# Performance work log

Hardware: AMD Instinct MI355X
Metric: run time of the kernel (lower is better)

## Reference

```python
import jax, jax.numpy as jnp
import numpy as np

EMBED_DIM = 1024
NUM_HEADS = 16
HEAD_DIM = EMBED_DIM // NUM_HEADS
FEATURE_EPS = 1e-06
DEN_EPS = 1e-06


def setup_inputs() -> dict:
    key = jax.random.key(0)
    k_x, k_qw, k_qb, k_ow, k_ob = jax.random.split(key, 5)
    b, l = 2, 2048
    x = jax.random.normal(k_x, (b, l, EMBED_DIM), dtype=jnp.float32)
    s = 1.0 / np.sqrt(EMBED_DIM)
    qkv_w = jax.random.uniform(k_qw, (3 * EMBED_DIM, EMBED_DIM), minval=-s, maxval=s, dtype=jnp.float32)
    qkv_b = jax.random.uniform(k_qb, (3 * EMBED_DIM,), minval=-s, maxval=s, dtype=jnp.float32)
    out_w = jax.random.uniform(k_ow, (EMBED_DIM, EMBED_DIM), minval=-s, maxval=s, dtype=jnp.float32)
    out_b = jax.random.uniform(k_ob, (EMBED_DIM,), minval=-s, maxval=s, dtype=jnp.float32)
    return {"x": x, "qkv_w": qkv_w, "qkv_b": qkv_b, "out_w": out_w, "out_b": out_b}


def reference(x, qkv_w, qkv_b, out_w, out_b):
    b, l, e = x.shape
    # qkv projection -> (3, b, h, l, d)
    qkv = (x @ qkv_w.T + qkv_b).reshape(b, l, 3, NUM_HEADS, HEAD_DIM)
    qkv = jnp.transpose(qkv, (2, 0, 3, 1, 4))
    q, k, v = qkv[0], qkv[1], qkv[2]
    # phi(x) = relu(x) + eps
    q = jax.nn.relu(q) + FEATURE_EPS
    k = jax.nn.relu(k) + FEATURE_EPS
    # running outer-product state: (b, h, l, d, d)
    kv = jnp.cumsum(jnp.einsum('bhld,bhle->bhlde', k, v), axis=2)
    k_cum = jnp.cumsum(k, axis=2)
    num = jnp.einsum('bhld,bhlde->bhle', q, kv)
    den = jnp.maximum(jnp.einsum('bhld,bhld->bhl', q, k_cum)[..., None], DEN_EPS)
    out = num / den  # (b, h, l, d)
    out = jnp.transpose(out, (0, 2, 1, 3)).reshape(b, l, e)
    return out @ out_w.T + out_b
```

## Files before the change

### kernel.cpp

```cpp
#include <hip/hip_runtime.h>
#include <hip/hip_bf16.h>
#include <cstdint>

#define B_ 2
#define L_ 2048
#define E_ 1024
#define H_ 16
#define D_ 64
#define N3_ 3072
#define NCHUNK 32
#define CHUNK 64

typedef __attribute__((ext_vector_type(8))) short bf16x8;
typedef __attribute__((ext_vector_type(4))) float f32x4;

__device__ __forceinline__ unsigned short f2bf(float f) {
  unsigned u = __float_as_uint(f);
  unsigned r = (u + 0x7fffu + ((u >> 16) & 1u)) >> 16;
  return (unsigned short)r;
}

__global__ __launch_bounds__(256) void k_cvt_bf16(const float* __restrict__ src,
                                                  unsigned short* __restrict__ dst,
                                                  int n4) {
  const int i = blockIdx.x * 256 + threadIdx.x;
  if (i < n4) {
    float4 v = reinterpret_cast<const float4*>(src)[i];
    ushort4 o;
    o.x = f2bf(v.x); o.y = f2bf(v.y); o.z = f2bf(v.z); o.w = f2bf(v.w);
    reinterpret_cast<ushort4*>(dst)[i] = o;
  }
}

template <int EPI>
__global__ __launch_bounds__(256) void k_mfma_gemm(
    const unsigned short* __restrict__ A,
    const unsigned short* __restrict__ Bm,
    const float* __restrict__ bias,
    float* __restrict__ O,
    unsigned short* __restrict__ Qb, unsigned short* __restrict__ Kb,
    unsigned short* __restrict__ Vb, const int K) {
  __shared__ short As[128 * 32];
  __shared__ short Bs[128 * 32];
  const int tid = threadIdx.x;
  const int lane = tid & 63;
  const int wave = tid >> 6;
  const int wr = wave >> 1, wc = wave & 1;
  const int m0 = blockIdx.y * 128, n0 = blockIdx.x * 128;
  const int srow = tid >> 2;
  const int scol = (tid & 3) << 3;
  f32x4 acc[4][4];
#pragma unroll
  for (int i = 0; i < 4; ++i)
#pragma unroll
    for (int j = 0; j < 4; ++j) acc[i][j] = (f32x4){0.f, 0.f, 0.f, 0.f};

  const int l15 = lane & 15, l16 = lane >> 4;
  const int aoff0 = (wr * 64 + l15) * 32 + l16 * 8;
  const int boff0 = (wc * 64 + l15) * 32 + l16 * 8;

  for (int k0 = 0; k0 < K; k0 += 32) {
    const short* gA = (const short*)&A[(size_t)(m0 + srow) * K + k0 + scol];
    const short* gB = (const short*)&Bm[(size_t)(n0 + srow) * K + k0 + scol];
    __builtin_amdgcn_global_load_lds(
        (const __attribute__((address_space(1))) unsigned int*)gA,
        (__attribute__((address_space(3))) unsigned int*)&As[tid * 8], 16, 0, 0);
    __builtin_amdgcn_global_load_lds(
        (const __attribute__((address_space(1))) unsigned int*)(gA + (size_t)64 * K),
        (__attribute__((address_space(3))) unsigned int*)&As[2048 + tid * 8], 16, 0, 0);
    __builtin_amdgcn_global_load_lds(
        (const __attribute__((address_space(1))) unsigned int*)gB,
        (__attribute__((address_space(3))) unsigned int*)&Bs[tid * 8], 16, 0, 0);
    __builtin_amdgcn_global_load_lds(
        (const __attribute__((address_space(1))) unsigned int*)(gB + (size_t)64 * K),
        (__attribute__((address_space(3))) unsigned int*)&Bs[2048 + tid * 8], 16, 0, 0);
    __syncthreads();
    bf16x8 af[4], bfr[4];
#pragma unroll
    for (int f = 0; f < 4; ++f)
      af[f] = *reinterpret_cast<const bf16x8*>(&As[aoff0 + f * 16 * 32]);
#pragma unroll
    for (int f = 0; f < 4; ++f)
      bfr[f] = *reinterpret_cast<const bf16x8*>(&Bs[boff0 + f * 16 * 32]);
#pragma unroll
    for (int m = 0; m < 4; ++m)
#pragma unroll
      for (int n = 0; n < 4; ++n)
        acc[m][n] = __builtin_amdgcn_mfma_f32_16x16x32_bf16(af[m], bfr[n], acc[m][n], 0, 0, 0);
    __syncthreads();
  }

  const int rbase = l16 * 4;
#pragma unroll
  for (int m = 0; m < 4; ++m) {
#pragma unroll
    for (int n = 0; n < 4; ++n) {
      const int col = n0 + wc * 64 + n * 16 + l15;
      const float bv = bias[col];
#pragma unroll
      for (int j = 0; j < 4; ++j) {
        const int row = m0 + wr * 64 + m * 16 + rbase + j;
        const float val = acc[m][n][j] + bv;
        if (EPI == 0) {
          const int b = row >> 11, l = row & 2047;
          const int t = col >> 10, hd = col & 1023;
          const int h = hd >> 6, d = hd & 63;
          const size_t dst = (((size_t)(b * 16 + h)) * 2048 + l) * 64 + d;
          if (t == 0)      Qb[dst] = f2bf(fmaxf(val, 0.f) + 1e-6f);
          else if (t == 1) Kb[dst] = f2bf(fmaxf(val, 0.f) + 1e-6f);
          else             Vb[dst] = f2bf(val);
        } else {
          O[(size_t)row * 1024 + col] = val;
        }
      }
    }
  }
}

__global__ __launch_bounds__(128) void k_chunkB(
    const unsigned short* __restrict__ Kb, const unsigned short* __restrict__ Vb,
    float* __restrict__ ST, unsigned short* __restrict__ Vtb) {
  __shared__ __align__(16) unsigned short Kt[64 * 72];
  __shared__ __align__(16) unsigned short Vt[64 * 72];
  const int tid = threadIdx.x;
  const int lane = tid & 63, w = tid >> 6;
  const int c = lane & 15, g = lane >> 4;
  const int bid = blockIdx.x;
  const int bh = bid >> 5, ch = bid & 31;
  const size_t base = ((size_t)bh * L_ + (size_t)ch * CHUNK) * D_;
  const int l = tid >> 1, hf = tid & 1;
  bf16x8 kv[4], vv[4];
#pragma unroll
  for (int i = 0; i < 4; ++i) {
    kv[i] = *reinterpret_cast<const bf16x8*>(&Kb[base + (size_t)l * 64 + hf * 32 + i * 8]);
    vv[i] = *reinterpret_cast<const bf16x8*>(&Vb[base + (size_t)l * 64 + hf * 32 + i * 8]);
  }
#pragma unroll
  for (int i = 0; i < 4; ++i)
#pragma unroll
    for (int r = 0; r < 8; ++r) {
      const int d = hf * 32 + i * 8 + r;
      Kt[d * 72 + l] = (unsigned short)kv[i][r];
      Vt[d * 72 + l] = (unsigned short)vv[i][r];
    }
  __syncthreads();
  bf16x8 kf[4][2], vf[2][2];
#pragma unroll
  for (int dt = 0; dt < 4; ++dt)
#pragma unroll
    for (int kh = 0; kh < 2; ++kh)
      kf[dt][kh] = *reinterpret_cast<const bf16x8*>(&Kt[(dt * 16 + c) * 72 + g * 8 + kh * 32]);
#pragma unroll
  for (int ei = 0; ei < 2; ++ei)
#pragma unroll
    for (int kh = 0; kh < 2; ++kh)
      vf[ei][kh] = *reinterpret_cast<const bf16x8*>(&Vt[((w * 2 + ei) * 16 + c) * 72 + g * 8 + kh * 32]);
  f32x4 acc[2][4];
#pragma unroll
  for (int ei = 0; ei < 2; ++ei)
#pragma unroll
    for (int dt = 0; dt < 4; ++dt) acc[ei][dt] = (f32x4){0.f, 0.f, 0.f, 0.f};
#pragma unroll
  for (int ei = 0; ei < 2; ++ei)
#pragma unroll
    for (int dt = 0; dt < 4; ++dt)
#pragma unroll
      for (int kh = 0; kh < 2; ++kh)
        acc[ei][dt] = __builtin_amdgcn_mfma_f32_16x16x32_bf16(vf[ei][kh], kf[dt][kh], acc[ei][dt], 0, 0, 0);
  const size_t stbase = (size_t)bid * 5120;
#pragma unroll
  for (int ei = 0; ei < 2; ++ei)
#pragma unroll
    for (int dt = 0; dt < 4; ++dt)
#pragma unroll
      for (int r = 0; r < 4; ++r)
        ST[stbase + (size_t)((w * 2 + ei) * 16 + 4 * g + r) * 64 + dt * 16 + c] = acc[ei][dt][r];
#pragma unroll
  for (int ei = 0; ei < 2; ++ei)
#pragma unroll
    for (int kh = 0; kh < 2; ++kh)
      *reinterpret_cast<bf16x8*>(&Vtb[(size_t)bid * 4096 + ((w * 2 + ei) * 16 + c) * 64 + g * 8 + kh * 32]) = vf[ei][kh];
  if (w == 0) {
    const short one = (c == 0) ? (short)0x3F80 : (short)0;
    bf16x8 of;
#pragma unroll
    for (int r = 0; r < 8; ++r) of[r] = one;
    f32x4 az[4];
#pragma unroll
    for (int dt = 0; dt < 4; ++dt) az[dt] = (f32x4){0.f, 0.f, 0.f, 0.f};
#pragma unroll
    for (int dt = 0; dt < 4; ++dt)
#pragma unroll
      for (int kh = 0; kh < 2; ++kh)
        az[dt] = __builtin_amdgcn_mfma_f32_16x16x32_bf16(of, kf[dt][kh], az[dt], 0, 0, 0);
    if (g == 0) {
#pragma unroll
      for (int dt = 0; dt < 4; ++dt)
        ST[stbase + 64 * 64 + dt * 16 + c] = az[dt][0];
    }
  }
}

__global__ __launch_bounds__(256) void k_prefix2(const float* __restrict__ ST,
                                                 unsigned short* __restrict__ STb) {
  const int bh = blockIdx.x;
  const int tid = threadIdx.x;
  float run[16];
#pragma unroll
  for (int j = 0; j < 16; ++j) run[j] = 0.f;
  for (int cc = 0; cc < NCHUNK; ++cc) {
    const size_t base = ((size_t)bh * NCHUNK + cc) * 5120;
    const float* p = ST + base + (size_t)tid * 16;
    unsigned short* qo = STb + base + (size_t)tid * 16;
#pragma unroll
    for (int j4 = 0; j4 < 4; ++j4) {
      float4 t = *reinterpret_cast<const float4*>(&p[j4 * 4]);
      ushort4 o;
      o.x = f2bf(run[j4 * 4 + 0]); o.y = f2bf(run[j4 * 4 + 1]);
      o.z = f2bf(run[j4 * 4 + 2]); o.w = f2bf(run[j4 * 4 + 3]);
      *reinterpret_cast<ushort4*>(&qo[j4 * 4]) = o;
      run[j4 * 4 + 0] += t.x; run[j4 * 4 + 1] += t.y;
      run[j4 * 4 + 2] += t.z; run[j4 * 4 + 3] += t.w;
    }
  }
  if (tid < 64) {
    float rz = 0.f;
    for (int cc = 0; cc < NCHUNK; ++cc) {
      const size_t base = ((size_t)bh * NCHUNK + cc) * 5120 + 4096 + tid;
      float t = ST[base];
      STb[base] = f2bf(rz);
      rz += t;
    }
  }
}

__global__ __launch_bounds__(256) void k_chunkD(
    const unsigned short* __restrict__ Qb, const unsigned short* __restrict__ Kb,
    const unsigned short* __restrict__ Vtb, const unsigned short* __restrict__ STb,
    unsigned short* __restrict__ attnb) {
  __shared__ __align__(16) unsigned short P[4][1024];
  const int tid = threadIdx.x;
  const int lane = tid & 63, lt = tid >> 6;
  const int c = lane & 15, g = lane >> 4;
  const int bid = blockIdx.x;
  const int bh = bid >> 5, ch = bid & 31;
  const int b = bh >> 4, h = bh & 15;
  const size_t qkbase = ((size_t)bh * L_ + (size_t)ch * CHUNK) * D_;
  bf16x8 q[2], k4[4][2], s[5][2], vt[4][2], pa[2];
#pragma unroll
  for (int kh = 0; kh < 2; ++kh)
    q[kh] = *reinterpret_cast<const bf16x8*>(&Qb[qkbase + (size_t)(lt * 16 + c) * 64 + g * 8 + kh * 32]);
#pragma unroll
  for (int jt = 0; jt < 4; ++jt)
#pragma unroll
    for (int kh = 0; kh < 2; ++kh)
      k4[jt][kh] = *reinterpret_cast<const bf16x8*>(&Kb[qkbase + (size_t)(jt * 16 + c) * 64 + g * 8 + kh * 32]);
  const size_t stbase = (size_t)bid * 5120;
#pragma unroll
  for (int et = 0; et < 5; ++et)
#pragma unroll
    for (int kh = 0; kh < 2; ++kh)
      s[et][kh] = *reinterpret_cast<const bf16x8*>(&STb[stbase + (size_t)(et * 16 + c) * 64 + g * 8 + kh * 32]);
#pragma unroll
  for (int et = 0; et < 4; ++et)
#pragma unroll
    for (int kh = 0; kh < 2; ++kh)
      vt[et][kh] = *reinterpret_cast<const bf16x8*>(&Vtb[(size_t)bid * 4096 + (size_t)(et * 16 + c) * 64 + g * 8 + kh * 32]);

  char* Pb = (char*)&P[lt][0];
  const int swz = (c & 7) << 4;
#pragma unroll
  for (int jt = 0; jt < 4; ++jt) {
    unsigned pk0 = 0, pk1 = 0;
    if (jt <= lt) {
      f32x4 a1 = (f32x4){0.f, 0.f, 0.f, 0.f};
#pragma unroll
      for (int kh = 0; kh < 2; ++kh)
        a1 = __builtin_amdgcn_mfma_f32_16x16x32_bf16(k4[jt][kh], q[kh], a1, 0, 0, 0);
      if (jt == lt) {
#pragma unroll
        for (int r = 0; r < 4; ++r) a1[r] = (4 * g + r <= c) ? a1[r] : 0.f;
      }
      pk0 = (unsigned)f2bf(a1[0]) | ((unsigned)f2bf(a1[1]) << 16);
      pk1 = (unsigned)f2bf(a1[2]) | ((unsigned)f2bf(a1[3]) << 16);
    }
    *reinterpret_cast<unsigned*>(Pb + ((c * 128 + 32 * jt + 8 * g + 0) ^ swz)) = pk0;
    *reinterpret_cast<unsigned*>(Pb + ((c * 128 + 32 * jt + 8 * g + 4) ^ swz)) = pk1;
  }
#pragma unroll
  for (int kh = 0; kh < 2; ++kh)
    pa[kh] = *reinterpret_cast<const bf16x8*>(Pb + (c * 128 + ((16 * g + 64 * kh) ^ swz)));

  f32x4 acc2[5];
#pragma unroll
  for (int et = 0; et < 5; ++et) acc2[et] = (f32x4){0.f, 0.f, 0.f, 0.f};
  const short one = (c == 0) ? (short)0x3F80 : (short)0;
  bf16x8 of;
#pragma unroll
  for (int r = 0; r < 8; ++r) of[r] = one;
#pragma unroll
  for (int et = 0; et < 5; ++et) {
#pragma unroll
    for (int kh = 0; kh < 2; ++kh) {
      acc2[et] = __builtin_amdgcn_mfma_f32_16x16x32_bf16(q[kh], s[et][kh], acc2[et], 0, 0, 0);
      bf16x8 vv = (et < 4) ? vt[et][kh] : of;
      acc2[et] = __builtin_amdgcn_mfma_f32_16x16x32_bf16(pa[kh], vv, acc2[et], 0, 0, 0);
    }
  }
  float inv[4];
#pragma unroll
  for (int r = 0; r < 4; ++r) {
    float dv = __shfl(acc2[4][r], lane & 48, 64);
    inv[r] = 1.f / fmaxf(dv, 1e-6f);
  }
  const size_t obase = ((size_t)b * L_ + (size_t)ch * CHUNK + (size_t)lt * 16) * E_ + (size_t)h * 64;
#pragma unroll
  for (int et = 0; et < 4; ++et)
#pragma unroll
    for (int r = 0; r < 4; ++r)
      attnb[obase + (size_t)(4 * g + r) * E_ + et * 16 + c] = f2bf(acc2[et][r] * inv[r]);
}

extern "C" void kernel_launch(void* const* d_in, const int* in_sizes, int n_in,
                              void* d_out, int out_size, void* d_ws, size_t ws_size,
                              hipStream_t stream) {
  const float* x = (const float*)d_in[0];
  const float* qkv_w = (const float*)d_in[1];
  const float* qkv_b = (const float*)d_in[2];
  const float* out_w = (const float*)d_in[3];
  const float* out_b = (const float*)d_in[4];
  float* out = (float*)d_out;

  const size_t SZ = (size_t)B_ * H_ * L_ * D_;
  char* p = (char*)d_ws;
  unsigned short* Qb = (unsigned short*)p;    p += SZ * 2;
  unsigned short* Kb = (unsigned short*)p;    p += SZ * 2;
  unsigned short* Vb = (unsigned short*)p;    p += SZ * 2;
  unsigned short* Vtb = (unsigned short*)p;   p += (size_t)1024 * 4096 * 2;
  float* ST = (float*)p;                      p += (size_t)1024 * 5120 * 4;
  unsigned short* STb = (unsigned short*)p;   p += (size_t)1024 * 5120 * 2;
  unsigned short* xb = (unsigned short*)p;    p += SZ * 2;
  unsigned short* wqkv = (unsigned short*)p;  p += (size_t)N3_ * E_ * 2;
  unsigned short* wout = (unsigned short*)p;  p += (size_t)E_ * E_ * 2;
  unsigned short* attnb = (unsigned short*)p; p += SZ * 2;

  dim3 blk(256);
  k_cvt_bf16<<<dim3(4096), blk, 0, stream>>>(x, xb, 1048576);
  k_cvt_bf16<<<dim3(3072), blk, 0, stream>>>(qkv_w, wqkv, 786432);
  k_cvt_bf16<<<dim3(1024), blk, 0, stream>>>(out_w, wout, 262144);
  k_mfma_gemm<0><<<dim3(N3_ / 128, (B_ * L_) / 128), blk, 0, stream>>>(
      xb, wqkv, qkv_b, nullptr, Qb, Kb, Vb, E_);
  k_chunkB<<<dim3(1024), dim3(128), 0, stream>>>(Kb, Vb, ST, Vtb);
  k_prefix2<<<dim3(B_ * H_), blk, 0, stream>>>(ST, STb);
  k_chunkD<<<dim3(1024), blk, 0, stream>>>(Qb, Kb, Vtb, STb, attnb);
  k_mfma_gemm<1><<<dim3(E_ / 128, (B_ * L_) / 128), blk, 0, stream>>>(
      attnb, wout, out_b, out, nullptr, nullptr, nullptr, E_);
}
```

Baseline: 197.1 us.

## Add 256x256 pipelined QKV GEMM with direct-to-LDS loads and parallelize prefix scan

Replaces the 128x128 QKV projection GEMM with a 512-thread 256x256 tile kernel. It uses global_load_lds async copies into double-buffered, XOR-swizzled shared memory, interleaves staging with MFMA quadrants, and raises wave priority during the MFMA bursts. The aim is more data reuse and overlap of global loads with tensor math. Separately, the chunk prefix-sum kernel now uses one thread per state element across a 2D grid instead of 32 blocks, which gives it more parallelism. The new GEMM launches far fewer blocks (12x16), which risks lower occupancy and CU utilization, and its hand-placed barriers and waitcnts are fragile.

```diff
diff --git a/kernel.cpp b/kernel.cpp
--- a/kernel.cpp
+++ b/kernel.cpp
@@ -32,14 +32,125 @@
   }
 }
 
-template <int EPI>
-__global__ __launch_bounds__(256) void k_mfma_gemm(
+__global__ __launch_bounds__(512, 2) void k_gemm256_qkv(
     const unsigned short* __restrict__ A,
     const unsigned short* __restrict__ Bm,
     const float* __restrict__ bias,
-    float* __restrict__ O,
     unsigned short* __restrict__ Qb, unsigned short* __restrict__ Kb,
-    unsigned short* __restrict__ Vb, const int K) {
+    unsigned short* __restrict__ Vb) {
+  __shared__ short As[2][16384];
+  __shared__ short Bs[2][16384];
+  const int tid = threadIdx.x;
+  const int lane = tid & 63, wave = tid >> 6;
+  const int wm = wave >> 2, wn = wave & 3;
+  const int m0 = blockIdx.y * 256, n0 = blockIdx.x * 256;
+  const int srow = tid >> 3, scol = (tid & 7) * 8;
+  const int ssw = (srow & 7) * 8;
+  const int l15 = lane & 15, l16 = lane >> 4;
+  const int sw = (l15 & 7) * 8;
+  const int NT = 16;
+
+  f32x4 acc[8][4];
+#pragma unroll
+  for (int i = 0; i < 8; ++i)
+#pragma unroll
+    for (int j = 0; j < 4; ++j) acc[i][j] = (f32x4){0.f, 0.f, 0.f, 0.f};
+
+  auto stage = [&](short (&S)[2][16384], const unsigned short* G, int R0,
+                   int d, int h, int kt) {
+#pragma unroll
+    for (int i = 0; i < 2; ++i) {
+      const int r = h * 128 + i * 64 + srow;
+      const unsigned short* src = &G[(size_t)(R0 + r) * 1024 + kt * 64 + (scol ^ ssw)];
+      short* dst = &S[d][r * 64 + scol];
+      __builtin_amdgcn_global_load_lds(
+          (const __attribute__((address_space(1))) unsigned int*)src,
+          (__attribute__((address_space(3))) unsigned int*)dst, 16, 0, 0);
+    }
+  };
+  auto lda = [&](bf16x8 (&dv)[8], int d, int kh) {
+#pragma unroll
+    for (int mi = 0; mi < 8; ++mi) {
+      const int r = wm * 128 + mi * 16 + l15;
+      dv[mi] = *reinterpret_cast<const bf16x8*>(&As[d][r * 64 + ((l16 * 8 + kh * 32) ^ sw)]);
+    }
+  };
+  auto ldb = [&](bf16x8 (&dv)[4], int d, int kh) {
+#pragma unroll
+    for (int ni = 0; ni < 4; ++ni) {
+      const int r = wn * 64 + ni * 16 + l15;
+      dv[ni] = *reinterpret_cast<const bf16x8*>(&Bs[d][r * 64 + ((l16 * 8 + kh * 32) ^ sw)]);
+    }
+  };
+  auto quad = [&](const bf16x8 (&af)[8], const bf16x8 (&bf)[4], int nlo) {
+    __builtin_amdgcn_s_setprio(1);
+#pragma unroll
+    for (int mi = 0; mi < 8; ++mi)
+#pragma unroll
+      for (int nn = 0; nn < 2; ++nn)
+        acc[mi][nlo + nn] = __builtin_amdgcn_mfma_f32_16x16x32_bf16(
+            af[mi], bf[nlo + nn], acc[mi][nlo + nn], 0, 0, 0);
+    __builtin_amdgcn_s_setprio(0);
+  };
+
+  stage(As, A, m0, 0, 0, 0); stage(As, A, m0, 0, 1, 0);
+  stage(Bs, Bm, n0, 0, 0, 0); stage(Bs, Bm, n0, 0, 1, 0);
+  stage(As, A, m0, 1, 0, 1); stage(As, A, m0, 1, 1, 1);
+  asm volatile("s_waitcnt vmcnt(4)" ::: "memory");
+  __builtin_amdgcn_s_barrier();
+
+  bf16x8 af0[8], af1[8], bf0[4], bf1[4];
+  for (int t = 0; t < NT; ++t) {
+    const int d = t & 1;
+    lda(af0, d, 0); ldb(bf0, d, 0);
+    if (t + 1 < NT) stage(Bs, Bm, n0, d ^ 1, 0, t + 1);
+    __builtin_amdgcn_s_barrier();
+    asm volatile("s_waitcnt lgkmcnt(0)" ::: "memory");
+    __builtin_amdgcn_sched_barrier(0);
+    quad(af0, bf0, 0);
+    __builtin_amdgcn_s_barrier();
+    lda(af1, d, 1); ldb(bf1, d, 1);
+    if (t + 1 < NT) stage(Bs, Bm, n0, d ^ 1, 1, t + 1);
+    __builtin_amdgcn_s_barrier();
+    asm volatile("s_waitcnt lgkmcnt(0)" ::: "memory");
+    __builtin_amdgcn_sched_barrier(0);
+    quad(af0, bf0, 2);
+    __builtin_amdgcn_s_barrier();
+    if (t + 2 < NT) stage(As, A, m0, d, 0, t + 2);
+    quad(af1, bf1, 0);
+    __builtin_amdgcn_s_barrier();
+    if (t + 2 < NT) stage(As, A, m0, d, 1, t + 2);
+    quad(af1, bf1, 2);
+    if (t + 2 < NT) asm volatile("s_waitcnt vmcnt(4)" ::: "memory");
+    else            asm volatile("s_waitcnt vmcnt(0)" ::: "memory");
+    __builtin_amdgcn_s_barrier();
+  }
+
+#pragma unroll
+  for (int mi = 0; mi < 8; ++mi) {
+#pragma unroll
+    for (int ni = 0; ni < 4; ++ni) {
+      const int col = n0 + wn * 64 + ni * 16 + l15;
+      const float bv = bias[col];
+      const int t = col >> 10, hd = col & 1023;
+      const int h = hd >> 6, dd = hd & 63;
+#pragma unroll
+      for (int j = 0; j < 4; ++j) {
+        const int row = m0 + wm * 128 + mi * 16 + l16 * 4 + j;
+        const float val = acc[mi][ni][j] + bv;
+        const int b = row >> 11, l = row & 2047;
+        const size_t dst = (((size_t)(b * 16 + h)) * 2048 + l) * 64 + dd;
+        if (t == 0)      Qb[dst] = f2bf(fmaxf(val, 0.f) + 1e-6f);
+        else if (t == 1) Kb[dst] = f2bf(fmaxf(val, 0.f) + 1e-6f);
+        else             Vb[dst] = f2bf(val);
+      }
+    }
+  }
+}
+
+__global__ __launch_bounds__(256) void k_gemm_out(
+    const unsigned short* __restrict__ A, const unsigned short* __restrict__ Bm,
+    const float* __restrict__ bias, float* __restrict__ O, const int K) {
   __shared__ short As[128 * 32];
   __shared__ short Bs[128 * 32];
   const int tid = threadIdx.x;
@@ -100,18 +211,7 @@
 #pragma unroll
       for (int j = 0; j < 4; ++j) {
         const int row = m0 + wr * 64 + m * 16 + rbase + j;
-        const float val = acc[m][n][j] + bv;
-        if (EPI == 0) {
-          const int b = row >> 11, l = row & 2047;
-          const int t = col >> 10, hd = col & 1023;
-          const int h = hd >> 6, d = hd & 63;
-          const size_t dst = (((size_t)(b * 16 + h)) * 2048 + l) * 64 + d;
-          if (t == 0)      Qb[dst] = f2bf(fmaxf(val, 0.f) + 1e-6f);
-          else if (t == 1) Kb[dst] = f2bf(fmaxf(val, 0.f) + 1e-6f);
-          else             Vb[dst] = f2bf(val);
-        } else {
-          O[(size_t)row * 1024 + col] = val;
-        }
+        O[(size_t)row * 1024 + col] = acc[m][n][j] + bv;
       }
     }
   }
@@ -204,33 +304,14 @@
 __global__ __launch_bounds__(256) void k_prefix2(const float* __restrict__ ST,
                                                  unsigned short* __restrict__ STb) {
   const int bh = blockIdx.x;
-  const int tid = threadIdx.x;
-  float run[16];
-#pragma unroll
-  for (int j = 0; j < 16; ++j) run[j] = 0.f;
+  const int e = blockIdx.y * 256 + threadIdx.x;
+  if (e >= 4160) return;
+  const size_t base = (size_t)bh * NCHUNK * 5120 + e;
+  float run = 0.f;
   for (int cc = 0; cc < NCHUNK; ++cc) {
-    const size_t base = ((size_t)bh * NCHUNK + cc) * 5120;
-    const float* p = ST + base + (size_t)tid * 16;
-    unsigned short* qo = STb + base + (size_t)tid * 16;
-#pragma unroll
-    for (int j4 = 0; j4 < 4; ++j4) {
-      float4 t = *reinterpret_cast<const float4*>(&p[j4 * 4]);
-      ushort4 o;
-      o.x = f2bf(run[j4 * 4 + 0]); o.y = f2bf(run[j4 * 4 + 1]);
-      o.z = f2bf(run[j4 * 4 + 2]); o.w = f2bf(run[j4 * 4 + 3]);
-      *reinterpret_cast<ushort4*>(&qo[j4 * 4]) = o;
-      run[j4 * 4 + 0] += t.x; run[j4 * 4 + 1] += t.y;
-      run[j4 * 4 + 2] += t.z; run[j4 * 4 + 3] += t.w;
-    }
-  }
-  if (tid < 64) {
-    float rz = 0.f;
-    for (int cc = 0; cc < NCHUNK; ++cc) {
-      const size_t base = ((size_t)bh * NCHUNK + cc) * 5120 + 4096 + tid;
-      float t = ST[base];
-      STb[base] = f2bf(rz);
-      rz += t;
-    }
+    const float t = ST[base + (size_t)cc * 5120];
+    STb[base + (size_t)cc * 5120] = f2bf(run);
+    run += t;
   }
 }
 
@@ -348,11 +429,11 @@
   k_cvt_bf16<<<dim3(4096), blk, 0, stream>>>(x, xb, 1048576);
   k_cvt_bf16<<<dim3(3072), blk, 0, stream>>>(qkv_w, wqkv, 786432);
   k_cvt_bf16<<<dim3(1024), blk, 0, stream>>>(out_w, wout, 262144);
-  k_mfma_gemm<0><<<dim3(N3_ / 128, (B_ * L_) / 128), blk, 0, stream>>>(
-      xb, wqkv, qkv_b, nullptr, Qb, Kb, Vb, E_);
+  k_gemm256_qkv<<<dim3(N3_ / 256, (B_ * L_) / 256), dim3(512), 0, stream>>>(
+      xb, wqkv, qkv_b, Qb, Kb, Vb);
   k_chunkB<<<dim3(1024), dim3(128), 0, stream>>>(Kb, Vb, ST, Vtb);
-  k_prefix2<<<dim3(B_ * H_), blk, 0, stream>>>(ST, STb);
+  k_prefix2<<<dim3(32, 17), blk, 0, stream>>>(ST, STb);
   k_chunkD<<<dim3(1024), blk, 0, stream>>>(Qb, Kb, Vtb, STb, attnb);
-  k_mfma_gemm<1><<<dim3(E_ / 128, (B_ * L_) / 128), blk, 0, stream>>>(
-      attnb, wout, out_b, out, nullptr, nullptr, nullptr, E_);
-}
+  k_gemm_out<<<dim3(E_ / 128, (B_ * L_) / 128), blk, 0, stream>>>(
+      attnb, wout, out_b, out, E_);
+}
```

Measured after the change: 180.6 us. 8.4% less time.
